# Optimization experiments

Measured on AMD Instinct MI355X. Metric: run time of the kernel, lower is better.

## Reference

```python
import jax, jax.numpy as jnp
import numpy as np

B, S, EMB, HID, VOCAB = 64, 4096, 20, 20, 256
TEMPERATURE = 0.001


def setup_inputs():
    key = jax.random.key(0)
    ks = jax.random.split(key, 16)
    rn = lambda k, shape: jax.random.normal(k, shape, jnp.float32) * 0.1
    return {
        'inp': jax.random.randint(ks[0], (B, S, 2), 0, 2**31 - 1, dtype=jnp.int32),
        'h0': jnp.zeros((1, B, HID), jnp.float32),
        'c0': jnp.zeros((1, B, HID), jnp.float32),
        'pc_emb': rn(ks[1], (4, VOCAB, EMB)),
        'addr_emb': rn(ks[2], (4, VOCAB, EMB)),
        'enc_W': rn(ks[3], (EMB, 4 * EMB)),
        'enc_b': rn(ks[4], (EMB,)),
        'W_ih': rn(ks[5], (4 * HID, 2 * EMB)),
        'W_hh': rn(ks[6], (4 * HID, HID)),
        'b_ih': rn(ks[7], (4 * HID,)),
        'b_hh': rn(ks[8], (4 * HID,)),
        'dec_W': rn(ks[9], (4, VOCAB, HID)),
        'dec_b': rn(ks[10], (4, VOCAB)),
        'd1_W': rn(ks[11], (10, 3 * EMB)),
        'd1_b': rn(ks[12], (10,)),
        'd2_W': rn(ks[13], (2, 10)),
        'd2_b': rn(ks[14], (2,)),
    }


def _byte_embed(vals, tables):
    # vals: (B,S) int32; vectorized replacement for get_bytes_2d + 4 gathers
    shifts = jnp.array([24, 16, 8, 0], dtype=jnp.int32)  # big-endian byte order
    byts = (vals[..., None] >> shifts) & 0xFF            # (B,S,4)
    embs = [tables[i][byts[..., i]] for i in range(4)]   # each (B,S,EMB)
    return jnp.concatenate(embs, axis=-1)                # (B,S,4*EMB)


def reference(inp, h0, c0, pc_emb, addr_emb, enc_W, enc_b, W_ih, W_hh,
              b_ih, b_hh, dec_W, dec_b, d1_W, d1_b, d2_W, d2_b):
    encode = lambda x: jax.nn.sigmoid(x @ enc_W.T + enc_b)  # Encoder MLP
    pc_e = encode(_byte_embed(inp[:, :, 0], pc_emb))         # (B,S,EMB)
    ad_e = encode(_byte_embed(inp[:, :, 1], addr_emb))       # (B,S,EMB)
    emb = jnp.concatenate([pc_e, ad_e], axis=-1)             # (B,S,2*EMB)

    # get_distribution_vector: KDE sample mean -> deterministic expectation
    # (= mean of the fitted data); detached in the original (input.detach()).
    dist_vector = jax.lax.stop_gradient(jnp.mean(emb, axis=1))  # (B,2*EMB)

    # LSTM (torch gate order i,f,g,o)
    def step(carry, x_t):
        h, c = carry
        gates = x_t @ W_ih.T + b_ih + h @ W_hh.T + b_hh
        i, f, g, o = jnp.split(gates, 4, axis=-1)
        c = jax.nn.sigmoid(f) * c + jax.nn.sigmoid(i) * jnp.tanh(g)
        h = jax.nn.sigmoid(o) * jnp.tanh(c)
        return (h, c), None

    (h, _), _ = jax.lax.scan(step, (h0[0], c0[0]), jnp.swapaxes(emb, 0, 1))
    hidden = h[None]                                          # (1,B,HID)

    # Decoder_lstm: 4 heads; softmax over dim=1 of (1,B,V) == batch axis
    logits = jnp.einsum('obh,kvh->kobv', hidden, dec_W) + dec_b[:, None, None, :]
    probs = jax.nn.softmax(logits / TEMPERATURE, axis=2)      # (4,1,B,V)

    # get_freq_rec: probs[i] @ address_embeddings[i].weight, concat, encode
    byte_e = jnp.einsum('kobv,kve->obke', probs, addr_emb)    # (1,B,4,EMB)
    fe = encode(byte_e.reshape(1, inp.shape[0], 4 * EMB))[0]  # (B,EMB)
    fr_in = jnp.concatenate([fe, dist_vector], axis=-1)       # (B,3*EMB)
    freq_rec = jax.nn.relu(fr_in @ d1_W.T + d1_b) @ d2_W.T + d2_b  # (B,2)
    return probs, logits, freq_rec[:, 0], freq_rec[:, 1]
```

## Files before the change

### kernel.cpp

```cpp
#include <hip/hip_runtime.h>
#include <math.h>

#define BB 64
#define SS 4096
#define OF_G    0
#define OF_BG   40960
#define OF_DIST 41056
#define OF_HFIN 43616
#define OF_WS   44896
#define OF_X    48096
#define WS_NEEDED_FLOATS (OF_X + (size_t)BB * SS * 80 + 8 * 80)

#define L2E 1.4426950408889634f

typedef float v2f __attribute__((ext_vector_type(2)));

__device__ __forceinline__ float fast_rcp(float x) { return __builtin_amdgcn_rcpf(x); }
__device__ __forceinline__ float fast_exp2(float x) { return __builtin_amdgcn_exp2f(x); }
__device__ __forceinline__ float sigm_prec(float x) { return 1.0f / (1.0f + __expf(-x)); }
#define RL(v, m) __int_as_float(__builtin_amdgcn_readlane(__float_as_int(v), (m)))

__global__ __launch_bounds__(256) void k_init(const float* __restrict__ pc_emb,
    const float* __restrict__ addr_emb, const float* __restrict__ enc_W,
    const float* __restrict__ b_ih, const float* __restrict__ b_hh,
    const float* __restrict__ W_ih, float* __restrict__ ws) {
  int gid = blockIdx.x * 256 + threadIdx.x;
  if (gid < 2048) {
    int t = gid >> 10;
    int i = (gid >> 8) & 3;
    int byt = gid & 255;
    const float* tab = (t == 0 ? pc_emb : addr_emb) + (i * 256 + byt) * 20;
    float tv[20];
#pragma unroll
    for (int m = 0; m < 20; m++) tv[m] = tab[m];
    float* Grow = ws + OF_G + gid * 20;
#pragma unroll
    for (int j = 0; j < 20; j++) {
      float acc = 0.f;
#pragma unroll
      for (int m = 0; m < 20; m++) acc = fmaf(enc_W[j * 80 + i * 20 + m], tv[m], acc);
      Grow[j] = acc;
    }
  } else if (gid < 2048 + 80) {
    int g = gid - 2048;
    float sc = (g >= 40 && g < 60) ? (2.0f * L2E) : (-L2E);
    ws[OF_BG + g] = (b_ih[g] + b_hh[g]) * sc;
  } else if (gid < 2048 + 80 + 2560) {
    ws[OF_DIST + (gid - 2128)] = 0.f;
  } else if (gid < 2048 + 80 + 2560 + 3200) {
    int q = gid - 4688;
    int g = q / 40;
    float sc = (g >= 40 && g < 60) ? (2.0f * L2E) : (-L2E);
    ws[OF_WS + q] = W_ih[q] * sc;
  }
}

__global__ __launch_bounds__(64) void k_embed(const int* __restrict__ inp,
    const float* __restrict__ enc_b, float* __restrict__ ws) {
  __shared__ float lds[80 * 65];
  int b = blockIdx.x >> 6;
  int schunk = (blockIdx.x & 63) << 6;
  int t = threadIdx.x;
  int s = schunk + t;
  unsigned v0 = (unsigned)inp[(b * SS + s) * 2 + 0];
  unsigned v1 = (unsigned)inp[(b * SS + s) * 2 + 1];
  const float4* G4 = (const float4*)(ws + OF_G);
  float e[40];
#pragma unroll
  for (int st = 0; st < 2; st++) {
    unsigned v = (st == 0) ? v0 : v1;
    int by0 = (int)(v >> 24);
    int by1 = (int)((v >> 16) & 255u);
    int by2 = (int)((v >> 8) & 255u);
    int by3 = (int)(v & 255u);
    int r0 = ((st * 4 + 0) * 256 + by0) * 5;
    int r1 = ((st * 4 + 1) * 256 + by1) * 5;
    int r2 = ((st * 4 + 2) * 256 + by2) * 5;
    int r3 = ((st * 4 + 3) * 256 + by3) * 5;
    float4 acc[5];
#pragma unroll
    for (int p = 0; p < 5; p++) {
      float4 a = G4[r0 + p];
      float4 bq = G4[r1 + p];
      float4 cq = G4[r2 + p];
      float4 d = G4[r3 + p];
      acc[p] = make_float4(a.x + bq.x + cq.x + d.x, a.y + bq.y + cq.y + d.y,
                           a.z + bq.z + cq.z + d.z, a.w + bq.w + cq.w + d.w);
    }
    const float* af = (const float*)acc;
#pragma unroll
    for (int j = 0; j < 20; j++)
      e[st * 20 + j] = sigm_prec(enc_b[j] + af[j]);
  }
  const float* Wsc = ws + OF_WS;
  const float* bg = ws + OF_BG;
#pragma unroll 4
  for (int g = 0; g < 80; g++) {
    float a = bg[g];
#pragma unroll
    for (int d = 0; d < 40; d++) a = fmaf(Wsc[g * 40 + d], e[d], a);
    lds[g * 65 + t] = a;
  }
  __syncthreads();
  float4* XF4 = (float4*)(ws + OF_X) + (size_t)(b * SS + schunk) * 20;
#pragma unroll
  for (int it = 0; it < 20; it++) {
    int q = it * 64 + t;
    int tok = q / 20;
    int jf = q - tok * 20;
    float4 vv;
    vv.x = lds[(0  + jf) * 65 + tok];
    vv.y = lds[(20 + jf) * 65 + tok];
    vv.z = lds[(40 + jf) * 65 + tok];
    vv.w = lds[(60 + jf) * 65 + tok];
    XF4[q] = vv;
  }
  __syncthreads();
  float* eT = lds;
#pragma unroll
  for (int d = 0; d < 40; d++) eT[d * 66 + t] = e[d];
  __syncthreads();
  if (t < 40) {
    float ssum = 0.f;
#pragma unroll 8
    for (int tok = 0; tok < 64; tok++) ssum += eT[t * 66 + tok];
    atomicAdd(ws + OF_DIST + b * 40 + t, ssum);
  }
}

__global__ __launch_bounds__(64) void k_lstm(const float* __restrict__ h0,
    const float* __restrict__ c0, const float* __restrict__ W_hh,
    float* __restrict__ ws) {
  int b = blockIdx.x;
  int l = threadIdx.x;
  int j = (l & 31) < 20 ? (l & 31) : 19;
  v2f wif[20], wgo[20];
#pragma unroll
  for (int m = 0; m < 20; m++) {
    wif[m] = (v2f){W_hh[(0 * 20 + j) * 20 + m] * (-L2E),
                   W_hh[(1 * 20 + j) * 20 + m] * (-L2E)};
    wgo[m] = (v2f){W_hh[(2 * 20 + j) * 20 + m] * (2.0f * L2E),
                   W_hh[(3 * 20 + j) * 20 + m] * (-L2E)};
  }
  float h = h0[b * 20 + j];
  float cs = c0[b * 20 + j] * (2.0f * L2E);
  const float4* Xp = (const float4*)(ws + OF_X) + (size_t)b * SS * 20 + j;
  float4 xb[8];
#pragma unroll
  for (int p = 0; p < 8; p++) xb[p] = Xp[p * 20];
  const float4* Xq = Xp;
  for (int s = 0; s < SS; s += 8) {
#pragma unroll
    for (int u = 0; u < 8; u++) {
      float4 x4 = xb[u];
      xb[u] = Xq[(u + 8) * 20];
      float hm[20];
#pragma unroll
      for (int m = 0; m < 4; m++) hm[m] = RL(h, m);
      v2f aifA = (v2f){x4.x, x4.y};
      v2f agoA = (v2f){x4.z, x4.w};
      v2f aifB = (v2f){0.f, 0.f};
      v2f agoB = (v2f){0.f, 0.f};
#pragma unroll
      for (int m = 0; m < 10; m++) {
        hm[m + 4] = RL(h, m + 4);
        v2f hv = (v2f){hm[m], hm[m]};
        aifA = __builtin_elementwise_fma(wif[m], hv, aifA);
        agoA = __builtin_elementwise_fma(wgo[m], hv, agoA);
      }
#pragma unroll
      for (int m = 10; m < 20; m++) {
        if (m + 4 < 20) hm[m + 4] = RL(h, m + 4);
        v2f hv = (v2f){hm[m], hm[m]};
        aifB = __builtin_elementwise_fma(wif[m], hv, aifB);
        agoB = __builtin_elementwise_fma(wgo[m], hv, agoB);
      }
      v2f aif = aifA + aifB;
      v2f ago = agoA + agoB;
      float si = fast_rcp(1.0f + fast_exp2(aif.x));
      float sf = fast_rcp(1.0f + fast_exp2(aif.y));
      float tg = fmaf(-2.0f, fast_rcp(1.0f + fast_exp2(ago.x)), 1.0f);
      float so = fast_rcp(1.0f + fast_exp2(ago.y));
      float p2 = (si * tg) * (2.0f * L2E);
      cs = fmaf(sf, cs, p2);
      float tc = fmaf(-2.0f, fast_rcp(1.0f + fast_exp2(cs)), 1.0f);
      h = so * tc;
    }
    Xq += 8 * 20;
  }
  if (l < 20) ws[OF_HFIN + b * 20 + l] = h;
}

__global__ __launch_bounds__(256) void k_dec(const float* __restrict__ dec_W,
    const float* __restrict__ dec_b, float* __restrict__ out,
    const float* __restrict__ ws) {
  int wid = blockIdx.x * 4 + (threadIdx.x >> 6);
  int lane = threadIdx.x & 63;
  int k = wid >> 8;
  int v = wid & 255;
  const float* hp = ws + OF_HFIN + lane * 20;
  const float* wp = dec_W + (k * 256 + v) * 20;
  float l = dec_b[k * 256 + v];
#pragma unroll
  for (int jj = 0; jj < 20; jj++) l = fmaf(hp[jj], wp[jj], l);
  float x = l / 0.001f;
  float mx = x;
#pragma unroll
  for (int off = 32; off; off >>= 1) mx = fmaxf(mx, __shfl_xor(mx, off));
  float ex = __expf(x - mx);
  float sm = ex;
#pragma unroll
  for (int off = 32; off; off >>= 1) sm += __shfl_xor(sm, off);
  float p = ex / sm;
  int oidx = (k * 64 + lane) * 256 + v;
  out[oidx] = p;
  out[65536 + oidx] = l;
}

__global__ __launch_bounds__(128) void k_freq(const float* __restrict__ addr_emb,
    const float* __restrict__ enc_W, const float* __restrict__ enc_b,
    const float* __restrict__ d1_W, const float* __restrict__ d1_b,
    const float* __restrict__ d2_W, const float* __restrict__ d2_b,
    float* __restrict__ out, const float* __restrict__ ws) {
  __shared__ float be[80];
  __shared__ float fr[60];
  __shared__ float r1[10];
  int b = blockIdx.x;
  int t = threadIdx.x;
  if (t < 80) {
    int k = t / 20, e2 = t % 20;
    const float* pp = out + (k * 64 + b) * 256;
    const float* ap = addr_emb + (k * 256) * 20 + e2;
    float acc = 0.f;
#pragma unroll 8
    for (int v = 0; v < 256; v++) acc = fmaf(pp[v], ap[v * 20], acc);
    be[t] = acc;
  }
  __syncthreads();
  if (t < 20) {
    float acc = enc_b[t];
#pragma unroll
    for (int d = 0; d < 80; d++) acc = fmaf(enc_W[t * 80 + d], be[d], acc);
    fr[t] = 1.0f / (1.0f + __expf(-acc));
  } else if (t < 60) {
    fr[t] = ws[OF_DIST + b * 40 + (t - 20)] * (1.0f / 4096.0f);
  }
  __syncthreads();
  if (t < 10) {
    float acc = d1_b[t];
#pragma unroll
    for (int d = 0; d < 60; d++) acc = fmaf(d1_W[t * 60 + d], fr[d], acc);
    r1[t] = acc > 0.f ? acc : 0.f;
  }
  __syncthreads();
  if (t < 2) {
    float acc = d2_b[t];
#pragma unroll
    for (int r = 0; r < 10; r++) acc = fmaf(d2_W[t * 10 + r], r1[r], acc);
    out[131072 + t * 64 + b] = acc;
  }
}

extern "C" void kernel_launch(void* const* d_in, const int* in_sizes, int n_in,
                              void* d_out, int out_size, void* d_ws, size_t ws_size,
                              hipStream_t stream) {
  const int*   inp    = (const int*)  d_in[0];
  const float* h0     = (const float*)d_in[1];
  const float* c0     = (const float*)d_in[2];
  const float* pc_emb = (const float*)d_in[3];
  const float* addr_e = (const float*)d_in[4];
  const float* enc_W  = (const float*)d_in[5];
  const float* enc_b  = (const float*)d_in[6];
  const float* W_ih   = (const float*)d_in[7];
  const float* W_hh   = (const float*)d_in[8];
  const float* b_ih   = (const float*)d_in[9];
  const float* b_hh   = (const float*)d_in[10];
  const float* dec_W  = (const float*)d_in[11];
  const float* dec_b  = (const float*)d_in[12];
  const float* d1_W   = (const float*)d_in[13];
  const float* d1_b   = (const float*)d_in[14];
  const float* d2_W   = (const float*)d_in[15];
  const float* d2_b   = (const float*)d_in[16];
  float* out = (float*)d_out;
  float* ws  = (float*)d_ws;

  if (ws_size < WS_NEEDED_FLOATS * sizeof(float)) return;

  hipLaunchKernelGGL(k_init, dim3(31), dim3(256), 0, stream,
                     pc_emb, addr_e, enc_W, b_ih, b_hh, W_ih, ws);
  hipLaunchKernelGGL(k_embed, dim3(4096), dim3(64), 0, stream, inp, enc_b, ws);
  hipLaunchKernelGGL(k_lstm, dim3(64), dim3(64), 0, stream, h0, c0, W_hh, ws);
  hipLaunchKernelGGL(k_dec, dim3(256), dim3(256), 0, stream, dec_W, dec_b, out, ws);
  hipLaunchKernelGGL(k_freq, dim3(64), dim3(128), 0, stream,
                     addr_e, enc_W, enc_b, d1_W, d1_b, d2_W, d2_b, out, ws);
}
```

Baseline: 1.011 ms.

## Split LSTM gate pairs across wave halves and exchange via permlane32 swap

```diff
diff --git a/kernel.cpp b/kernel.cpp
--- a/kernel.cpp
+++ b/kernel.cpp
@@ -134,59 +134,65 @@
   int b = blockIdx.x;
   int l = threadIdx.x;
   int j = (l & 31) < 20 ? (l & 31) : 19;
-  v2f wif[20], wgo[20];
+  float q0 = (float)l, q1 = (float)l;
+  asm("v_permlane32_swap_b32 %0, %1" : "+v"(q0), "+v"(q1));
+  int dir = (__builtin_amdgcn_readfirstlane(__float_as_int(q0)) == 0) ? 0 : 1;
+  int sp = ((l >> 5) ^ dir) & 1;
+  v2f wAB[20];
 #pragma unroll
   for (int m = 0; m < 20; m++) {
-    wif[m] = (v2f){W_hh[(0 * 20 + j) * 20 + m] * (-L2E),
-                   W_hh[(1 * 20 + j) * 20 + m] * (-L2E)};
-    wgo[m] = (v2f){W_hh[(2 * 20 + j) * 20 + m] * (2.0f * L2E),
-                   W_hh[(3 * 20 + j) * 20 + m] * (-L2E)};
-  }
+    float wa = (sp == 0) ? W_hh[(0 * 20 + j) * 20 + m] * (-L2E)
+                         : W_hh[(2 * 20 + j) * 20 + m] * (2.0f * L2E);
+    float wb = (sp == 0) ? W_hh[(1 * 20 + j) * 20 + m] * (-L2E)
+                         : W_hh[(3 * 20 + j) * 20 + m] * (-L2E);
+    wAB[m] = (v2f){wa, wb};
+  }
+  v2f kA = (sp == 0) ? (v2f){1.0f, 1.0f} : (v2f){-4.0f * L2E, 1.0f};
+  v2f kB = (sp == 0) ? (v2f){0.0f, 0.0f} : (v2f){2.0f * L2E, 0.0f};
   float h = h0[b * 20 + j];
   float cs = c0[b * 20 + j] * (2.0f * L2E);
-  const float4* Xp = (const float4*)(ws + OF_X) + (size_t)b * SS * 20 + j;
-  float4 xb[8];
-#pragma unroll
-  for (int p = 0; p < 8; p++) xb[p] = Xp[p * 20];
-  const float4* Xq = Xp;
+  const float2* Xp = (const float2*)(ws + OF_X) + (size_t)b * SS * 40 + j * 2 + sp;
+  float2 xb[8];
+#pragma unroll
+  for (int p = 0; p < 8; p++) xb[p] = Xp[p * 40];
+  const float2* Xq = Xp;
   for (int s = 0; s < SS; s += 8) {
 #pragma unroll
     for (int u = 0; u < 8; u++) {
-      float4 x4 = xb[u];
-      xb[u] = Xq[(u + 8) * 20];
+      float2 x2 = xb[u];
+      xb[u] = Xq[(u + 8) * 40];
       float hm[20];
 #pragma unroll
       for (int m = 0; m < 4; m++) hm[m] = RL(h, m);
-      v2f aifA = (v2f){x4.x, x4.y};
-      v2f agoA = (v2f){x4.z, x4.w};
-      v2f aifB = (v2f){0.f, 0.f};
-      v2f agoB = (v2f){0.f, 0.f};
+      v2f aA = (v2f){x2.x, x2.y};
+      v2f aB = (v2f){0.f, 0.f};
 #pragma unroll
       for (int m = 0; m < 10; m++) {
         hm[m + 4] = RL(h, m + 4);
         v2f hv = (v2f){hm[m], hm[m]};
-        aifA = __builtin_elementwise_fma(wif[m], hv, aifA);
-        agoA = __builtin_elementwise_fma(wgo[m], hv, agoA);
+        aA = __builtin_elementwise_fma(wAB[m], hv, aA);
       }
 #pragma unroll
       for (int m = 10; m < 20; m++) {
         if (m + 4 < 20) hm[m + 4] = RL(h, m + 4);
         v2f hv = (v2f){hm[m], hm[m]};
-        aifB = __builtin_elementwise_fma(wif[m], hv, aifB);
-        agoB = __builtin_elementwise_fma(wgo[m], hv, agoB);
+        aB = __builtin_elementwise_fma(wAB[m], hv, aB);
       }
-      v2f aif = aifA + aifB;
-      v2f ago = agoA + agoB;
-      float si = fast_rcp(1.0f + fast_exp2(aif.x));
-      float sf = fast_rcp(1.0f + fast_exp2(aif.y));
-      float tg = fmaf(-2.0f, fast_rcp(1.0f + fast_exp2(ago.x)), 1.0f);
-      float so = fast_rcp(1.0f + fast_exp2(ago.y));
-      float p2 = (si * tg) * (2.0f * L2E);
-      cs = fmaf(sf, cs, p2);
+      v2f a = aA + aB;
+      float e0 = fast_exp2(a.x);
+      float e1 = fast_exp2(a.y);
+      v2f den = (v2f){1.0f + e0, 1.0f + e1};
+      v2f r = (v2f){fast_rcp(den.x), fast_rcp(den.y)};
+      v2f res = __builtin_elementwise_fma(r, kA, kB);
+      float d0 = res.x, s0 = res.x;
+      float d1 = res.y, s1 = res.y;
+      asm("v_permlane32_swap_b32 %0, %1" : "+v"(d0), "+v"(s0));
+      asm("v_permlane32_swap_b32 %0, %1" : "+v"(d1), "+v"(s1));
+      cs = fmaf(d1, cs, d0 * s0);
       float tc = fmaf(-2.0f, fast_rcp(1.0f + fast_exp2(cs)), 1.0f);
-      h = so * tc;
+      h = s1 * tc;
     }
-    Xq += 8 * 20;
+    Xq += 8 * 40;
   }
   if (l < 20) ws[OF_HFIN + b * 20 + l] = h;
 }
```

After: 867.0 us. 14.3% less time.
